# Optimization experiments

Hardware: AMD Instinct MI355X
Metric: run time of the kernel (lower is better)

Reference implementation:

```python
import jax, jax.numpy as jnp
import numpy as np

DT = 0.001
BATCH, INPUT_SIZE, HIDDEN_SIZE, T = 32, 16384, 1024, 10


def setup_inputs() -> dict:
    key = jax.random.key(0)
    k1, k2, k3 = jax.random.split(key, 3)
    input_spikes = (jax.random.uniform(k1, (BATCH, INPUT_SIZE, T)) < 0.1).astype(jnp.float32)
    weight = jax.random.normal(k2, (INPUT_SIZE, HIDDEN_SIZE), dtype=jnp.float32) * 0.1
    synaptic_strength = jnp.ones((INPUT_SIZE, HIDDEN_SIZE), jnp.float32)
    threshold = jnp.ones((HIDDEN_SIZE,), jnp.float32)  # threshold_init = 1.0
    firing_rate_estimate = jnp.zeros((HIDDEN_SIZE,), jnp.float32)
    return {
        "input_spikes": input_spikes,
        "weight": weight,
        "synaptic_strength": synaptic_strength,
        "threshold": threshold,
        "firing_rate_estimate": firing_rate_estimate,
        "tau_mem": jnp.float32(0.02),
        "tau_syn": jnp.float32(0.005),
        "target_rate": jnp.float32(0.1),
        "homeostatic_lr": jnp.float32(0.001),
        "time_steps": T,
    }


def reference(input_spikes, weight, synaptic_strength, threshold,
              firing_rate_estimate, tau_mem, tau_syn, target_rate,
              homeostatic_lr, time_steps):
    # input_spikes: [B, I, T]; eval mode (no stochastic STDP branch)
    B = input_spikes.shape[0]
    H = threshold.shape[0]
    alpha_mem = jnp.exp(-DT / tau_mem)
    alpha_syn = jnp.exp(-DT / tau_syn)
    # precompute the per-step weighted input once: [T, B, H]
    w_eff = weight * synaptic_strength
    weighted = jnp.einsum('bit,ih->tbh', input_spikes[..., :time_steps], w_eff)

    def step(carry, w_in):
        v, i, fre, thr = carry
        i = alpha_syn * i + w_in
        v = alpha_mem * v + i
        spikes = (v >= thr[None, :]).astype(v.dtype)
        v = v - spikes * thr[None, :]  # reset_mode='subtract'
        spike_rate = spikes.mean(axis=0)
        fre = 0.99 * fre + 0.01 * spike_rate
        thr = thr + homeostatic_lr * (fre - target_rate)  # homeostatic adaptation
        diag = (v.mean(), spike_rate.mean(), thr.mean())
        return (v, i, fre, thr), (spikes, diag)

    init = (jnp.zeros((B, H), input_spikes.dtype),
            jnp.zeros((B, H), input_spikes.dtype),
            firing_rate_estimate, threshold)
    _, (spikes_tbh, (mem_means, rate_means, thr_means)) = jax.lax.scan(step, init, weighted)
    output_spikes = jnp.transpose(spikes_tbh, (1, 2, 0))  # [B, H, T]
    return output_spikes, mem_means, rate_means, thr_means
```

## Files before the change

### kernel.cpp

```cpp
#include <hip/hip_runtime.h>
#include <stdint.h>

#define B_ 32
#define I_ 16384
#define H_ 1024
#define T_ 10
#define M_ 320

typedef __attribute__((ext_vector_type(8))) short short8;
typedef __attribute__((ext_vector_type(4))) float f32x4;
typedef __attribute__((ext_vector_type(4))) unsigned int u32x4;

__global__ __launch_bounds__(256) void pack_s(const float* __restrict__ spikes,
                                              uint16_t* __restrict__ Sbf) {
  __shared__ uint16_t tile[M_ * 72];
  const int i0 = blockIdx.x * 64;
  for (int u = threadIdx.x; u < 32 * 640; u += 256) {
    int b = u / 640;
    int pos = u - b * 640;
    int il = pos / 10;
    int t = pos - il * 10;
    float val = spikes[(size_t)b * (I_ * T_) + (size_t)i0 * T_ + pos];
    union { float f; unsigned int u; } cv; cv.f = val;
    tile[(t * 32 + b) * 72 + il] = (uint16_t)(cv.u >> 16);
  }
  __syncthreads();
  for (int u = threadIdx.x; u < M_ * 8; u += 256) {
    int m = u >> 3;
    int il8 = u & 7;
    u32x4 w = *(const u32x4*)&tile[m * 72 + il8 * 8];
    *(u32x4*)&Sbf[(size_t)m * I_ + i0 + il8 * 8] = w;
  }
}

__global__ __launch_bounds__(256) void gemm(const uint16_t* __restrict__ Sbf,
                                            const float* __restrict__ Wg,
                                            const float* __restrict__ Sg,
                                            float* __restrict__ partial,
                                            int kchunk) {
  __shared__ uint16_t A_lds[M_ * 56];
  __shared__ unsigned int W_lds[64 * 36];

  const int nt = blockIdx.x & 15;
  const int ks = blockIdx.x >> 4;
  const int n0 = nt * 64;
  const int tid = threadIdx.x;
  const int lane = tid & 63, wid = tid >> 6;
  const int quad = lane >> 4, l15 = lane & 15;

  f32x4 acc[5][4];
#pragma unroll
  for (int a = 0; a < 5; a++)
#pragma unroll
    for (int b = 0; b < 4; b++) acc[a][b] = f32x4{0.f, 0.f, 0.f, 0.f};

  unsigned int* A32 = (unsigned int*)A_lds;
  const int stages = kchunk >> 5;
  const int kofs = ks * kchunk;
  const int wn = tid & 63;
  const int wko = tid >> 6;

  for (int s = 0; s < stages; ++s) {
    const int kbase = kofs + (s << 5);
    __syncthreads();
    {
      u32x4 av[5];
#pragma unroll
      for (int p = 0; p < 5; p++) {
        int f16 = p * 256 + tid;
        int m = f16 >> 2, kq = f16 & 3;
        av[p] = *(const u32x4*)&Sbf[(size_t)m * I_ + kbase + kq * 8];
      }
#pragma unroll
      for (int p = 0; p < 5; p++) {
        int f16 = p * 256 + tid;
        int m = f16 >> 2, kq = f16 & 3;
        *(u32x4*)&A32[m * 28 + kq * 4] = av[p];
      }
    }
    {
      unsigned int words[8];
#pragma unroll
      for (int p = 0; p < 8; p++) {
        int kl = 8 * wko + p;
        size_t g = (size_t)(kbase + kl) * H_ + n0 + wn;
        float w = Wg[g] * Sg[g];
        union { float f; unsigned int u; } cv; cv.f = w;
        unsigned int hb = (cv.u + 0x7FFFu + ((cv.u >> 16) & 1u)) >> 16;
        union { unsigned int u; float f; } hv; hv.u = hb << 16;
        float lo = w - hv.f;
        union { float f; unsigned int u; } cl; cl.f = lo;
        unsigned int lb = (cl.u + 0x7FFFu + ((cl.u >> 16) & 1u)) >> 16;
        words[p] = hb | (lb << 16);
      }
      u32x4 w0 = {words[0], words[1], words[2], words[3]};
      u32x4 w1 = {words[4], words[5], words[6], words[7]};
      *(u32x4*)&W_lds[wn * 36 + 8 * wko] = w0;
      *(u32x4*)&W_lds[wn * 36 + 8 * wko + 4] = w1;
    }
    __syncthreads();
    short8 af[5];
#pragma unroll
    for (int tm = 0; tm < 5; tm++) {
      int m = wid * 80 + tm * 16 + l15;
      af[tm] = *(const short8*)&A32[m * 28 + quad * 4];
    }
#pragma unroll
    for (int tn = 0; tn < 4; tn++) {
      int n = tn * 16 + l15;
      u32x4 r0 = *(const u32x4*)&W_lds[n * 36 + quad * 8];
      u32x4 r1 = *(const u32x4*)&W_lds[n * 36 + quad * 8 + 4];
      u32x4 hu, lu;
      hu.x = (r0.x & 0xffffu) | (r0.y << 16);
      hu.y = (r0.z & 0xffffu) | (r0.w << 16);
      hu.z = (r1.x & 0xffffu) | (r1.y << 16);
      hu.w = (r1.z & 0xffffu) | (r1.w << 16);
      lu.x = (r0.x >> 16) | (r0.y & 0xffff0000u);
      lu.y = (r0.z >> 16) | (r0.w & 0xffff0000u);
      lu.z = (r1.x >> 16) | (r1.y & 0xffff0000u);
      lu.w = (r1.z >> 16) | (r1.w & 0xffff0000u);
      short8 bhi = __builtin_bit_cast(short8, hu);
      short8 blo = __builtin_bit_cast(short8, lu);
#pragma unroll
      for (int tm = 0; tm < 5; tm++) {
        acc[tm][tn] = __builtin_amdgcn_mfma_f32_16x16x32_bf16(af[tm], bhi,
                                                              acc[tm][tn], 0, 0, 0);
        acc[tm][tn] = __builtin_amdgcn_mfma_f32_16x16x32_bf16(af[tm], blo,
                                                              acc[tm][tn], 0, 0, 0);
      }
    }
  }
#pragma unroll
  for (int tm = 0; tm < 5; tm++)
#pragma unroll
    for (int tn = 0; tn < 4; tn++) {
      int mrow = wid * 80 + tm * 16 + quad * 4;
      int ncol = n0 + tn * 16 + l15;
      float* dst = partial + ((size_t)ks * M_ + mrow) * H_ + ncol;
      dst[0 * H_] = acc[tm][tn].x;
      dst[1 * H_] = acc[tm][tn].y;
      dst[2 * H_] = acc[tm][tn].z;
      dst[3 * H_] = acc[tm][tn].w;
    }
}

__global__ __launch_bounds__(256) void reduce_w(const float* __restrict__ partial,
                                                float* __restrict__ weighted,
                                                int KS) {
  int j = (blockIdx.x * 256 + threadIdx.x) * 4;
  f32x4 s = f32x4{0.f, 0.f, 0.f, 0.f};
  for (int k = 0; k < KS; k++) {
    f32x4 p = *(const f32x4*)&partial[(size_t)k * (M_ * H_) + j];
    s += p;
  }
  *(f32x4*)&weighted[j] = s;
}

__global__ __launch_bounds__(1024) void scan(const float* __restrict__ weighted,
                                             const float* __restrict__ threshold,
                                             const float* __restrict__ fre0,
                                             const float* __restrict__ p_tau_mem,
                                             const float* __restrict__ p_tau_syn,
                                             const float* __restrict__ p_target,
                                             const float* __restrict__ p_lr,
                                             float* __restrict__ out) {
  __shared__ float red[32 * 33];
  __shared__ float thr_sh[32];
  const int tid = threadIdx.x;
  const int hl = tid & 31, b = tid >> 5;
  const int h = blockIdx.x * 32 + hl;
  const float alpha_mem = expf(-0.001f / p_tau_mem[0]);
  const float alpha_syn = expf(-0.001f / p_tau_syn[0]);
  const float target = p_target[0], lr = p_lr[0];
  float v = 0.f, isyn = 0.f;
  float fre = fre0[h];
  float thr = threshold[h];
  if (b == 0) thr_sh[hl] = thr;
  __syncthreads();
  for (int t = 0; t < T_; t++) {
    float w_in = weighted[(size_t)(t * 32 + b) * H_ + h];
    isyn = alpha_syn * isyn + w_in;
    v = alpha_mem * v + isyn;
    float thc = thr_sh[hl];
    float spike = (v >= thc) ? 1.f : 0.f;
    v -= spike * thc;
    out[(size_t)b * (H_ * T_) + (size_t)h * T_ + t] = spike;
    red[b * 33 + hl] = spike;
    __syncthreads();
    for (int s2 = 16; s2 >= 1; s2 >>= 1) {
      if (b < s2) red[b * 33 + hl] += red[(b + s2) * 33 + hl];
      __syncthreads();
    }
    float rate = (b == 0) ? red[hl] * (1.f / 32.f) : 0.f;
    __syncthreads();
    red[b * 33 + hl] = v;
    __syncthreads();
    for (int s2 = 16; s2 >= 1; s2 >>= 1) {
      if (b < s2) red[b * 33 + hl] += red[(b + s2) * 33 + hl];
      __syncthreads();
    }
    if (b == 0) {
      fre = 0.99f * fre + 0.01f * rate;
      thr = thr + lr * (fre - target);
      thr_sh[hl] = thr;
      float vs = red[hl];
      float rs = rate, ts = thr;
      for (int off = 16; off >= 1; off >>= 1) {
        vs += __shfl_down(vs, off, 32);
        rs += __shfl_down(rs, off, 32);
        ts += __shfl_down(ts, off, 32);
      }
      if (hl == 0) {
        atomicAdd(&out[327680 + t], vs * (1.f / 32768.f));
        atomicAdd(&out[327690 + t], rs * (1.f / 1024.f));
        atomicAdd(&out[327700 + t], ts * (1.f / 1024.f));
      }
    }
    __syncthreads();
  }
}

extern "C" void kernel_launch(void* const* d_in, const int* in_sizes, int n_in,
                              void* d_out, int out_size, void* d_ws, size_t ws_size,
                              hipStream_t stream) {
  const float* spikes    = (const float*)d_in[0];
  const float* weight    = (const float*)d_in[1];
  const float* strength  = (const float*)d_in[2];
  const float* threshold = (const float*)d_in[3];
  const float* fre0      = (const float*)d_in[4];
  const float* tau_mem   = (const float*)d_in[5];
  const float* tau_syn   = (const float*)d_in[6];
  const float* target    = (const float*)d_in[7];
  const float* lr        = (const float*)d_in[8];
  float* out = (float*)d_out;

  const size_t sbf_bytes = (size_t)M_ * I_ * 2;
  const size_t slice     = (size_t)M_ * H_ * 4;
  int KS = 16;
  while (KS > 1 && sbf_bytes + (size_t)(KS + 1) * slice > ws_size) KS >>= 1;

  uint16_t* Sbf   = (uint16_t*)d_ws;
  float* partial  = (float*)((char*)d_ws + sbf_bytes);
  float* weighted = (float*)((char*)d_ws + sbf_bytes + (size_t)KS * slice);

  pack_s<<<I_ / 64, 256, 0, stream>>>(spikes, Sbf);
  gemm<<<16 * KS, 256, 0, stream>>>(Sbf, weight, strength, partial, I_ / KS);
  reduce_w<<<(M_ * H_) / 1024, 256, 0, stream>>>(partial, weighted, KS);
  hipMemsetAsync(out + 327680, 0, 30 * sizeof(float), stream);
  scan<<<H_ / 32, 1024, 0, stream>>>(weighted, threshold, fre0, tau_mem, tau_syn,
                                     target, lr, out);
}
```

Before: 246.9 us.

## Split GEMM over M tiles, vectorize loads, swizzle W LDS, per-thread scan

The GEMM now splits the 320-row M dimension into three 128-row tiles, so it launches three times as many blocks with fewer accumulators each, and occupancy is hinted at 3. Weight and strength are loaded as float4 and written into a k-swizzled LDS layout to cut bank conflicts. The pack kernel uses vectorized float4 loads with a smaller tile. The scan is rewritten so each thread handles one hidden unit across all 32 batch rows in registers, replacing the LDS tree reductions and block barriers with wavefront shuffles. The cost is that the last M tile is partly padding, and W is reloaded once per M tile.

```diff
diff --git a/kernel.cpp b/kernel.cpp
--- a/kernel.cpp
+++ b/kernel.cpp
@@ -6,6 +6,7 @@
 #define H_ 1024
 #define T_ 10
 #define M_ 320
+#define MT_ 128
 
 typedef __attribute__((ext_vector_type(8))) short short8;
 typedef __attribute__((ext_vector_type(4))) float f32x4;
@@ -13,103 +14,110 @@
 
 __global__ __launch_bounds__(256) void pack_s(const float* __restrict__ spikes,
                                               uint16_t* __restrict__ Sbf) {
-  __shared__ uint16_t tile[M_ * 72];
-  const int i0 = blockIdx.x * 64;
-  for (int u = threadIdx.x; u < 32 * 640; u += 256) {
-    int b = u / 640;
-    int pos = u - b * 640;
-    int il = pos / 10;
-    int t = pos - il * 10;
-    float val = spikes[(size_t)b * (I_ * T_) + (size_t)i0 * T_ + pos];
-    union { float f; unsigned int u; } cv; cv.f = val;
-    tile[(t * 32 + b) * 72 + il] = (uint16_t)(cv.u >> 16);
+  __shared__ uint16_t tile[M_ * 40];
+  const int i0 = blockIdx.x * 32;
+#pragma unroll
+  for (int p = 0; p < 10; p++) {
+    int e = p * 256 + threadIdx.x;
+    int b = e / 80;
+    int r = e - b * 80;
+    f32x4 val = *(const f32x4*)&spikes[(size_t)b * (I_ * T_) + (size_t)i0 * T_ + r * 4];
+#pragma unroll
+    for (int j = 0; j < 4; j++) {
+      int pos = r * 4 + j;
+      int il = pos / 10;
+      int t = pos - il * 10;
+      float f = (j == 0) ? val.x : (j == 1) ? val.y : (j == 2) ? val.z : val.w;
+      union { float f; unsigned int u; } cv; cv.f = f;
+      tile[(t * 32 + b) * 40 + il] = (uint16_t)(cv.u >> 16);
+    }
   }
   __syncthreads();
-  for (int u = threadIdx.x; u < M_ * 8; u += 256) {
-    int m = u >> 3;
-    int il8 = u & 7;
-    u32x4 w = *(const u32x4*)&tile[m * 72 + il8 * 8];
+#pragma unroll
+  for (int p = 0; p < 5; p++) {
+    int e = p * 256 + threadIdx.x;
+    int m = e >> 2, il8 = e & 3;
+    u32x4 w = *(const u32x4*)&tile[m * 40 + il8 * 8];
     *(u32x4*)&Sbf[(size_t)m * I_ + i0 + il8 * 8] = w;
   }
 }
 
-__global__ __launch_bounds__(256) void gemm(const uint16_t* __restrict__ Sbf,
-                                            const float* __restrict__ Wg,
-                                            const float* __restrict__ Sg,
-                                            float* __restrict__ partial,
-                                            int kchunk) {
-  __shared__ uint16_t A_lds[M_ * 56];
+__global__ __launch_bounds__(256, 3) void gemm(const uint16_t* __restrict__ Sbf,
+                                               const float* __restrict__ Wg,
+                                               const float* __restrict__ Sg,
+                                               float* __restrict__ partial,
+                                               int kchunk) {
+  __shared__ uint16_t A_lds[MT_ * 56];
   __shared__ unsigned int W_lds[64 * 36];
 
-  const int nt = blockIdx.x & 15;
-  const int ks = blockIdx.x >> 4;
+  const int bid = blockIdx.x;
+  const int mt = bid % 3;
+  const int rest = bid / 3;
+  const int nt = rest & 15;
+  const int ks = rest >> 4;
+  const int mbase = mt * MT_;
   const int n0 = nt * 64;
   const int tid = threadIdx.x;
   const int lane = tid & 63, wid = tid >> 6;
   const int quad = lane >> 4, l15 = lane & 15;
 
-  f32x4 acc[5][4];
-#pragma unroll
-  for (int a = 0; a < 5; a++)
+  f32x4 acc[2][4];
+#pragma unroll
+  for (int a = 0; a < 2; a++)
 #pragma unroll
     for (int b = 0; b < 4; b++) acc[a][b] = f32x4{0.f, 0.f, 0.f, 0.f};
 
   unsigned int* A32 = (unsigned int*)A_lds;
   const int stages = kchunk >> 5;
   const int kofs = ks * kchunk;
-  const int wn = tid & 63;
-  const int wko = tid >> 6;
 
   for (int s = 0; s < stages; ++s) {
     const int kbase = kofs + (s << 5);
     __syncthreads();
-    {
-      u32x4 av[5];
-#pragma unroll
-      for (int p = 0; p < 5; p++) {
-        int f16 = p * 256 + tid;
-        int m = f16 >> 2, kq = f16 & 3;
-        av[p] = *(const u32x4*)&Sbf[(size_t)m * I_ + kbase + kq * 8];
-      }
-#pragma unroll
-      for (int p = 0; p < 5; p++) {
-        int f16 = p * 256 + tid;
-        int m = f16 >> 2, kq = f16 & 3;
-        *(u32x4*)&A32[m * 28 + kq * 4] = av[p];
-      }
-    }
-    {
-      unsigned int words[8];
-#pragma unroll
-      for (int p = 0; p < 8; p++) {
-        int kl = 8 * wko + p;
-        size_t g = (size_t)(kbase + kl) * H_ + n0 + wn;
-        float w = Wg[g] * Sg[g];
-        union { float f; unsigned int u; } cv; cv.f = w;
+#pragma unroll
+    for (int p = 0; p < 2; p++) {
+      int e = p * 256 + tid;
+      int m = e >> 2, kq = e & 3;
+      int mg = mbase + m;
+      u32x4 av = u32x4{0u, 0u, 0u, 0u};
+      if (mg < M_) av = *(const u32x4*)&Sbf[(size_t)mg * I_ + kbase + kq * 8];
+      *(u32x4*)&A32[m * 28 + kq * 4] = av;
+    }
+#pragma unroll
+    for (int p = 0; p < 2; p++) {
+      int e = p * 256 + tid;
+      int k = e >> 4;
+      int nq = e & 15;
+      size_t g = (size_t)(kbase + k) * H_ + n0 + nq * 4;
+      f32x4 wv = *(const f32x4*)&Wg[g];
+      f32x4 sv = *(const f32x4*)&Sg[g];
+      float prod[4] = {wv.x * sv.x, wv.y * sv.y, wv.z * sv.z, wv.w * sv.w};
+      int pblk = ((k >> 2) ^ (nq & 7)) << 2;
+      int koff = pblk + (k & 3);
+#pragma unroll
+      for (int j = 0; j < 4; j++) {
+        union { float f; unsigned int u; } cv; cv.f = prod[j];
         unsigned int hb = (cv.u + 0x7FFFu + ((cv.u >> 16) & 1u)) >> 16;
         union { unsigned int u; float f; } hv; hv.u = hb << 16;
-        float lo = w - hv.f;
+        float lo = prod[j] - hv.f;
         union { float f; unsigned int u; } cl; cl.f = lo;
         unsigned int lb = (cl.u + 0x7FFFu + ((cl.u >> 16) & 1u)) >> 16;
-        words[p] = hb | (lb << 16);
+        W_lds[(nq * 4 + j) * 36 + koff] = hb | (lb << 16);
       }
-      u32x4 w0 = {words[0], words[1], words[2], words[3]};
-      u32x4 w1 = {words[4], words[5], words[6], words[7]};
-      *(u32x4*)&W_lds[wn * 36 + 8 * wko] = w0;
-      *(u32x4*)&W_lds[wn * 36 + 8 * wko + 4] = w1;
     }
     __syncthreads();
-    short8 af[5];
-#pragma unroll
-    for (int tm = 0; tm < 5; tm++) {
-      int m = wid * 80 + tm * 16 + l15;
+    short8 af[2];
+#pragma unroll
+    for (int tm = 0; tm < 2; tm++) {
+      int m = wid * 32 + tm * 16 + l15;
       af[tm] = *(const short8*)&A32[m * 28 + quad * 4];
     }
 #pragma unroll
     for (int tn = 0; tn < 4; tn++) {
       int n = tn * 16 + l15;
-      u32x4 r0 = *(const u32x4*)&W_lds[n * 36 + quad * 8];
-      u32x4 r1 = *(const u32x4*)&W_lds[n * 36 + quad * 8 + 4];
+      int gsw = (n >> 2) & 7;
+      u32x4 r0 = *(const u32x4*)&W_lds[n * 36 + (((2 * quad) ^ gsw) << 2)];
+      u32x4 r1 = *(const u32x4*)&W_lds[n * 36 + (((2 * quad + 1) ^ gsw) << 2)];
       u32x4 hu, lu;
       hu.x = (r0.x & 0xffffu) | (r0.y << 16);
       hu.y = (r0.z & 0xffffu) | (r0.w << 16);
@@ -122,7 +130,7 @@
       short8 bhi = __builtin_bit_cast(short8, hu);
       short8 blo = __builtin_bit_cast(short8, lu);
 #pragma unroll
-      for (int tm = 0; tm < 5; tm++) {
+      for (int tm = 0; tm < 2; tm++) {
         acc[tm][tn] = __builtin_amdgcn_mfma_f32_16x16x32_bf16(af[tm], bhi,
                                                               acc[tm][tn], 0, 0, 0);
         acc[tm][tn] = __builtin_amdgcn_mfma_f32_16x16x32_bf16(af[tm], blo,
@@ -131,16 +139,18 @@
     }
   }
 #pragma unroll
-  for (int tm = 0; tm < 5; tm++)
+  for (int tm = 0; tm < 2; tm++)
 #pragma unroll
     for (int tn = 0; tn < 4; tn++) {
-      int mrow = wid * 80 + tm * 16 + quad * 4;
-      int ncol = n0 + tn * 16 + l15;
-      float* dst = partial + ((size_t)ks * M_ + mrow) * H_ + ncol;
-      dst[0 * H_] = acc[tm][tn].x;
-      dst[1 * H_] = acc[tm][tn].y;
-      dst[2 * H_] = acc[tm][tn].z;
-      dst[3 * H_] = acc[tm][tn].w;
+      int mrow = mbase + wid * 32 + tm * 16 + quad * 4;
+      if (mrow < M_) {
+        int ncol = n0 + tn * 16 + l15;
+        float* dst = partial + ((size_t)ks * M_ + mrow) * H_ + ncol;
+        dst[0 * H_] = acc[tm][tn].x;
+        dst[1 * H_] = acc[tm][tn].y;
+        dst[2 * H_] = acc[tm][tn].z;
+        dst[3 * H_] = acc[tm][tn].w;
+      }
     }
 }
 
@@ -156,67 +166,51 @@
   *(f32x4*)&weighted[j] = s;
 }
 
-__global__ __launch_bounds__(1024) void scan(const float* __restrict__ weighted,
-                                             const float* __restrict__ threshold,
-                                             const float* __restrict__ fre0,
-                                             const float* __restrict__ p_tau_mem,
-                                             const float* __restrict__ p_tau_syn,
-                                             const float* __restrict__ p_target,
-                                             const float* __restrict__ p_lr,
-                                             float* __restrict__ out) {
-  __shared__ float red[32 * 33];
-  __shared__ float thr_sh[32];
-  const int tid = threadIdx.x;
-  const int hl = tid & 31, b = tid >> 5;
-  const int h = blockIdx.x * 32 + hl;
+__global__ __launch_bounds__(64) void scan(const float* __restrict__ weighted,
+                                           const float* __restrict__ threshold,
+                                           const float* __restrict__ fre0,
+                                           const float* __restrict__ p_tau_mem,
+                                           const float* __restrict__ p_tau_syn,
+                                           const float* __restrict__ p_target,
+                                           const float* __restrict__ p_lr,
+                                           float* __restrict__ out) {
+  const int h = blockIdx.x * 64 + threadIdx.x;
   const float alpha_mem = expf(-0.001f / p_tau_mem[0]);
   const float alpha_syn = expf(-0.001f / p_tau_syn[0]);
   const float target = p_target[0], lr = p_lr[0];
-  float v = 0.f, isyn = 0.f;
+  float v[B_], isyn[B_];
+#pragma unroll
+  for (int b = 0; b < B_; b++) { v[b] = 0.f; isyn[b] = 0.f; }
   float fre = fre0[h];
   float thr = threshold[h];
-  if (b == 0) thr_sh[hl] = thr;
-  __syncthreads();
   for (int t = 0; t < T_; t++) {
-    float w_in = weighted[(size_t)(t * 32 + b) * H_ + h];
-    isyn = alpha_syn * isyn + w_in;
-    v = alpha_mem * v + isyn;
-    float thc = thr_sh[hl];
-    float spike = (v >= thc) ? 1.f : 0.f;
-    v -= spike * thc;
-    out[(size_t)b * (H_ * T_) + (size_t)h * T_ + t] = spike;
-    red[b * 33 + hl] = spike;
-    __syncthreads();
-    for (int s2 = 16; s2 >= 1; s2 >>= 1) {
-      if (b < s2) red[b * 33 + hl] += red[(b + s2) * 33 + hl];
-      __syncthreads();
-    }
-    float rate = (b == 0) ? red[hl] * (1.f / 32.f) : 0.f;
-    __syncthreads();
-    red[b * 33 + hl] = v;
-    __syncthreads();
-    for (int s2 = 16; s2 >= 1; s2 >>= 1) {
-      if (b < s2) red[b * 33 + hl] += red[(b + s2) * 33 + hl];
-      __syncthreads();
-    }
-    if (b == 0) {
-      fre = 0.99f * fre + 0.01f * rate;
-      thr = thr + lr * (fre - target);
-      thr_sh[hl] = thr;
-      float vs = red[hl];
-      float rs = rate, ts = thr;
-      for (int off = 16; off >= 1; off >>= 1) {
-        vs += __shfl_down(vs, off, 32);
-        rs += __shfl_down(rs, off, 32);
-        ts += __shfl_down(ts, off, 32);
-      }
-      if (hl == 0) {
-        atomicAdd(&out[327680 + t], vs * (1.f / 32768.f));
-        atomicAdd(&out[327690 + t], rs * (1.f / 1024.f));
-        atomicAdd(&out[327700 + t], ts * (1.f / 1024.f));
-      }
-    }
-    __syncthreads();
+    float rsum = 0.f, vsum = 0.f;
+#pragma unroll
+    for (int b = 0; b < B_; b++) {
+      float w_in = weighted[(size_t)(t * 32 + b) * H_ + h];
+      isyn[b] = alpha_syn * isyn[b] + w_in;
+      v[b] = alpha_mem * v[b] + isyn[b];
+      float spike = (v[b] >= thr) ? 1.f : 0.f;
+      v[b] -= spike * thr;
+      out[(size_t)b * (H_ * T_) + (size_t)h * T_ + t] = spike;
+      rsum += spike;
+      vsum += v[b];
+    }
+    float rate = rsum * (1.f / 32.f);
+    fre = 0.99f * fre + 0.01f * rate;
+    thr = thr + lr * (fre - target);
+    float rr = rate, vv = vsum, tt = thr;
+#pragma unroll
+    for (int off = 32; off >= 1; off >>= 1) {
+      rr += __shfl_xor(rr, off);
+      vv += __shfl_xor(vv, off);
+      tt += __shfl_xor(tt, off);
+    }
+    if (threadIdx.x == 0) {
+      atomicAdd(&out[327680 + t], vv * (1.f / 32768.f));
+      atomicAdd(&out[327690 + t], rr * (1.f / 1024.f));
+      atomicAdd(&out[327700 + t], tt * (1.f / 1024.f));
+    }
   }
 }
 
@@ -243,10 +237,10 @@
   float* partial  = (float*)((char*)d_ws + sbf_bytes);
   float* weighted = (float*)((char*)d_ws + sbf_bytes + (size_t)KS * slice);
 
-  pack_s<<<I_ / 64, 256, 0, stream>>>(spikes, Sbf);
-  gemm<<<16 * KS, 256, 0, stream>>>(Sbf, weight, strength, partial, I_ / KS);
+  pack_s<<<I_ / 32, 256, 0, stream>>>(spikes, Sbf);
+  gemm<<<3 * 16 * KS, 256, 0, stream>>>(Sbf, weight, strength, partial, I_ / KS);
   reduce_w<<<(M_ * H_) / 1024, 256, 0, stream>>>(partial, weighted, KS);
   hipMemsetAsync(out + 327680, 0, 30 * sizeof(float), stream);
-  scan<<<H_ / 32, 1024, 0, stream>>>(weighted, threshold, fre0, tau_mem, tau_syn,
-                                     target, lr, out);
-}
+  scan<<<H_ / 64, 64, 0, stream>>>(weighted, threshold, fre0, tau_mem, tau_syn,
+                                   target, lr, out);
+}
```

New measurement: 273.8 us. 1.11x slower.
